# Performance work log

Measured on AMD Instinct MI355X. Metric: run time of the kernel, lower is better.

## Reference

```python
import jax, jax.numpy as jnp
import numpy as np
import math

B, S, D, H = 4, 1024, 512, 8
HD = D // H
HID = 4 * D


def clinear(xr, xi, lm, ph, bm=None, bp=None):
    # magnitude-phase parameterized complex linear: W = exp(lm) * e^{i*ph}
    mag = jnp.exp(lm)
    wr = mag * jnp.cos(ph)
    wi = mag * jnp.sin(ph)
    r = xr @ wr.T - xi @ wi.T
    i = xr @ wi.T + xi @ wr.T
    if bm is not None:
        r = r + bm * jnp.cos(bp)
        i = i + bm * jnp.sin(bp)
    return r, i


def cln(xr, xi, gr, gi, br, bi, eps=1e-6):
    mr = xr.mean(-1, keepdims=True)
    mi = xi.mean(-1, keepdims=True)
    cr, ci = xr - mr, xi - mi
    var = (cr * cr + ci * ci).mean(-1, keepdims=True)
    inv = 1.0 / jnp.sqrt(var + eps)
    nr, ni = cr * inv, ci * inv
    return nr * gr - ni * gi + br, nr * gi + ni * gr + bi


def rotate_half(x):
    h = x.shape[-1] // 2
    return jnp.concatenate([-x[..., h:], x[..., :h]], axis=-1)


def split_heads(x):  # (B,S,D) -> (B,H,S,HD)
    return x.reshape(B, S, H, HD).transpose(0, 2, 1, 3)


def merge_heads(x):  # (B,H,S,HD) -> (B,S,D)
    return x.transpose(0, 2, 1, 3).reshape(B, S, D)


def setup_inputs() -> dict:
    key = jax.random.key(0)
    ks = iter(jax.random.split(key, 64))

    def lin(o_f, i_f):
        lm = jax.random.normal(next(ks), (o_f, i_f)) * 0.1 - 0.5 * math.log(i_f)
        ph = jax.random.uniform(next(ks), (o_f, i_f), minval=-math.pi, maxval=math.pi)
        return lm.astype(jnp.float32), ph.astype(jnp.float32)

    inp = {}
    inp['x_real'] = jax.random.normal(next(ks), (B, S, D), dtype=jnp.float32)
    inp['x_imag'] = jax.random.normal(next(ks), (B, S, D), dtype=jnp.float32)
    inp['ln1_gr'] = jnp.ones(D); inp['ln1_gi'] = jnp.zeros(D)
    inp['ln1_br'] = jnp.zeros(D); inp['ln1_bi'] = jnp.zeros(D)
    for nm in ['q', 'k', 'v', 'o']:
        lm, ph = lin(D, D)
        inp[nm + '_lm'] = lm; inp[nm + '_ph'] = ph
        inp[nm + '_bm'] = jnp.zeros(D); inp[nm + '_bp'] = jnp.zeros(D)
    inp['ln2_gr'] = jnp.ones(D); inp['ln2_gi'] = jnp.zeros(D)
    inp['ln2_br'] = jnp.zeros(D); inp['ln2_bi'] = jnp.zeros(D)
    inp['gate_lm'], inp['gate_ph'] = lin(HID, D)
    inp['up_lm'], inp['up_ph'] = lin(HID, D)
    inp['down_lm'], inp['down_ph'] = lin(D, HID)
    return inp


def reference(x_real, x_imag, ln1_gr, ln1_gi, ln1_br, ln1_bi,
              q_lm, q_ph, q_bm, q_bp, k_lm, k_ph, k_bm, k_bp,
              v_lm, v_ph, v_bm, v_bp, o_lm, o_ph, o_bm, o_bp,
              ln2_gr, ln2_gi, ln2_br, ln2_bi,
              gate_lm, gate_ph, up_lm, up_ph, down_lm, down_ph):
    # --- pre-attention complex LayerNorm ---
    hr, hi = cln(x_real, x_imag, ln1_gr, ln1_gi, ln1_br, ln1_bi)

    # --- complex QKV projections ---
    qr, qi = clinear(hr, hi, q_lm, q_ph, q_bm, q_bp)
    kr, ki = clinear(hr, hi, k_lm, k_ph, k_bm, k_bp)
    vr, vi = clinear(hr, hi, v_lm, v_ph, v_bm, v_bp)
    qr, qi = split_heads(qr), split_heads(qi)
    kr, ki = split_heads(kr), split_heads(ki)
    vr, vi = split_heads(vr), split_heads(vi)

    # --- complex RoPE (same real rotation applied to real & imag parts) ---
    pos = jnp.arange(S, dtype=jnp.float32)
    inv_freq = 1.0 / (10000.0 ** (jnp.arange(0, HD, 2, dtype=jnp.float32) / HD))
    freqs = pos[:, None] * inv_freq[None, :]          # (S, HD/2)
    cos = jnp.concatenate([jnp.cos(freqs)] * 2, -1)[None, None]  # (1,1,S,HD)
    sin = jnp.concatenate([jnp.sin(freqs)] * 2, -1)[None, None]
    rot = lambda x: x * cos + rotate_half(x) * sin
    qr, qi, kr, ki = rot(qr), rot(qi), rot(kr), rot(ki)

    # --- Hermitian attention: Re(q . conj(k)) = qr.kr + qi.ki ---
    scale = 1.0 / math.sqrt(HD)
    scores = (jnp.einsum('bhqd,bhkd->bhqk', qr, kr)
              + jnp.einsum('bhqd,bhkd->bhqk', qi, ki)) * scale
    causal = jnp.tril(jnp.ones((S, S), dtype=bool))
    scores = jnp.where(causal, scores, jnp.float32(-1e9))
    attn = jax.nn.softmax(scores, axis=-1)            # real-valued weights
    ar = jnp.einsum('bhqk,bhkd->bhqd', attn, vr)
    ai = jnp.einsum('bhqk,bhkd->bhqd', attn, vi)
    ar, ai = merge_heads(ar), merge_heads(ai)
    ar, ai = clinear(ar, ai, o_lm, o_ph, o_bm, o_bp)

    # --- residual + LN2 ---
    res_r, res_i = x_real + ar, x_imag + ai
    hr, hi = cln(res_r, res_i, ln2_gr, ln2_gi, ln2_br, ln2_bi)

    # --- complex gated FFN (SwiGLU-style, complex gating) ---
    gr_, gi_ = clinear(hr, hi, gate_lm, gate_ph)
    s = jax.nn.sigmoid(jnp.sqrt(gr_ * gr_ + gi_ * gi_))  # sigmoid(|gate|)
    gar, gai = gr_ * s, gi_ * s
    ur, ui = clinear(hr, hi, up_lm, up_ph)
    hid_r = gar * ur - gai * ui
    hid_i = gar * ui + gai * ur
    dr, di = clinear(hid_r, hid_i, down_lm, down_ph)

    out_r = res_r + dr
    out_i = res_i + di
    return jnp.stack([out_r, out_i], axis=0)  # (2, B, S, D)
```

## Files before the change

kernel.cpp:

```cpp
#include <hip/hip_runtime.h>
#include <math.h>

#define kB 4
#define kS 1024
#define kD 512
#define kH 8
#define kHD 64
#define kHID 2048
#define kNT (kB * kS)
#define kBSD (kNT * kD)

typedef __attribute__((ext_vector_type(8))) short bf16x8;
typedef __attribute__((ext_vector_type(4))) float f32x4;

#define AS1 __attribute__((address_space(1)))
#define AS3 __attribute__((address_space(3)))

__device__ __forceinline__ float bf2f(unsigned short u) {
  return __uint_as_float(((unsigned int)u) << 16);
}
__device__ __forceinline__ unsigned short f2bf(float f) {
  unsigned int u = __float_as_uint(f);
  u += 0x7fffu + ((u >> 16) & 1u);
  return (unsigned short)(u >> 16);
}
__device__ __forceinline__ unsigned int pack2(unsigned short a, unsigned short b) {
  return (unsigned)a | ((unsigned)b << 16);
}

__global__ __launch_bounds__(256) void build_wA_kernel(
    const float* __restrict__ qlm, const float* __restrict__ qph,
    const float* __restrict__ klm, const float* __restrict__ kph,
    const float* __restrict__ vlm, const float* __restrict__ vph,
    const float* __restrict__ olm, const float* __restrict__ oph,
    const float* __restrict__ qbm, const float* __restrict__ qbp,
    const float* __restrict__ kbm, const float* __restrict__ kbp,
    const float* __restrict__ vbm, const float* __restrict__ vbp,
    const float* __restrict__ obm, const float* __restrict__ obp,
    const float* __restrict__ xr, const float* __restrict__ xi,
    const float* __restrict__ g_r, const float* __restrict__ g_i,
    const float* __restrict__ b_r, const float* __restrict__ b_i,
    unsigned short* __restrict__ Wqkv, unsigned short* __restrict__ Wo,
    float* __restrict__ qkvBias, float* __restrict__ oBias,
    unsigned short* __restrict__ H) {
  int bx = blockIdx.x;
  if (bx >= 4104) {
    int w = threadIdx.x >> 6, lane = threadIdx.x & 63;
    int t = (bx - 4104) * 4 + w;
    int d0 = lane * 8;
    const float* xrt = xr + (size_t)t * 512 + d0;
    const float* xit = xi + (size_t)t * 512 + d0;
    float4 a0 = *(const float4*)&xrt[0];
    float4 a1 = *(const float4*)&xrt[4];
    float4 c0 = *(const float4*)&xit[0];
    float4 c1 = *(const float4*)&xit[4];
    float s1 = a0.x + a0.y + a0.z + a0.w + a1.x + a1.y + a1.z + a1.w;
    float s2 = c0.x + c0.y + c0.z + c0.w + c1.x + c1.y + c1.z + c1.w;
#pragma unroll
    for (int off = 1; off < 64; off <<= 1) {
      s1 += __shfl_xor(s1, off);
      s2 += __shfl_xor(s2, off);
    }
    float mr = s1 * (1.f / kD), mi = s2 * (1.f / kD);
    float ar[8] = {a0.x, a0.y, a0.z, a0.w, a1.x, a1.y, a1.z, a1.w};
    float ai[8] = {c0.x, c0.y, c0.z, c0.w, c1.x, c1.y, c1.z, c1.w};
    float v = 0.f;
#pragma unroll
    for (int e = 0; e < 8; e++) {
      float cr = ar[e] - mr, ci = ai[e] - mi;
      v += cr * cr + ci * ci;
    }
#pragma unroll
    for (int off = 1; off < 64; off <<= 1) v += __shfl_xor(v, off);
    float inv = rsqrtf(v * (1.f / kD) + 1e-6f);
    unsigned short pr[8], pi[8];
#pragma unroll
    for (int e = 0; e < 8; e++) {
      float nr = (ar[e] - mr) * inv;
      float ni = (ai[e] - mi) * inv;
      pr[e] = f2bf(nr * g_r[d0 + e] - ni * g_i[d0 + e] + b_r[d0 + e]);
      pi[e] = f2bf(nr * g_i[d0 + e] + ni * g_r[d0 + e] + b_i[d0 + e]);
    }
    unsigned short* ot = H + (size_t)t * 1024 + d0;
    *(bf16x8*)&ot[0] = *(const bf16x8*)pr;
    *(bf16x8*)&ot[512] = *(const bf16x8*)pi;
    return;
  }
  if (bx >= 4096) {
    int gid = (bx - 4096) * 256 + threadIdx.x;
    int seg = gid >> 9, m = gid & 511;
    const float* bm = seg == 0 ? qbm : seg == 1 ? kbm : seg == 2 ? vbm : obm;
    const float* bp = seg == 0 ? qbp : seg == 1 ? kbp : seg == 2 ? vbp : obp;
    float s, c;
    __sincosf(bp[m], &s, &c);
    float br = bm[m] * c, bi = bm[m] * s;
    if (seg < 3) {
      int h = m >> 6, d = m & 63;
      qkvBias[seg * 1024 + h * 128 + d] = br;
      qkvBias[seg * 1024 + h * 128 + 64 + d] = bi;
    } else {
      oBias[m] = br;
      oBias[512 + m] = bi;
    }
    return;
  }
  int gid = bx * 256 + threadIdx.x;
  int seg = gid >> 18;
  int id = gid & 262143;
  const float* lm = seg == 0 ? qlm : seg == 1 ? klm : seg == 2 ? vlm : olm;
  const float* ph = seg == 0 ? qph : seg == 1 ? kph : seg == 2 ? vph : oph;
  float mm = __expf(lm[id]);
  float s, c;
  __sincosf(ph[id], &s, &c);
  float wr = mm * c, wi = mm * s;
  int m = id >> 9, k = id & 511;
  if (seg < 3) {
    int h = m >> 6, d = m & 63;
    size_t rowR = (size_t)seg * 1024 + h * 128 + d;
    size_t rowI = rowR + 64;
    Wqkv[rowR * 1024 + k] = f2bf(wr);
    Wqkv[rowR * 1024 + 512 + k] = f2bf(-wi);
    Wqkv[rowI * 1024 + k] = f2bf(wi);
    Wqkv[rowI * 1024 + 512 + k] = f2bf(wr);
  } else {
    Wo[(size_t)m * 1024 + k] = f2bf(wr);
    Wo[(size_t)m * 1024 + 512 + k] = f2bf(-wi);
    Wo[(size_t)(512 + m) * 1024 + k] = f2bf(wi);
    Wo[(size_t)(512 + m) * 1024 + 512 + k] = f2bf(wr);
  }
}

__global__ __launch_bounds__(256) void build_wB_kernel(
    const float* __restrict__ glm, const float* __restrict__ gph,
    const float* __restrict__ ulm, const float* __restrict__ uph,
    const float* __restrict__ dlm, const float* __restrict__ dph,
    unsigned short* __restrict__ Wgu, unsigned short* __restrict__ Wd) {
  int gid = blockIdx.x * 256 + threadIdx.x;
  int seg = gid >> 19;
  int id0 = (gid & 524287) * 2;
  const float* lm = seg == 0 ? glm : seg == 1 ? ulm : dlm;
  const float* ph = seg == 0 ? gph : seg == 1 ? uph : dph;
  float2 lm2 = *(const float2*)&lm[id0];
  float2 ph2 = *(const float2*)&ph[id0];
  float m0 = __expf(lm2.x), m1 = __expf(lm2.y);
  float s0, c0, s1, c1;
  __sincosf(ph2.x, &s0, &c0);
  __sincosf(ph2.y, &s1, &c1);
  float wr0 = m0 * c0, wi0 = m0 * s0;
  float wr1 = m1 * c1, wi1 = m1 * s1;
  if (seg < 2) {
    int T = id0 >> 9, k = id0 & 511;
    size_t base = (size_t)(T >> 4) * 64 + (T & 15);
    size_t rR = base + (seg * 2 + 0) * 16;
    size_t rI = base + (seg * 2 + 1) * 16;
    *(unsigned int*)&Wgu[rR * 1024 + k] = pack2(f2bf(wr0), f2bf(wr1));
    *(unsigned int*)&Wgu[rR * 1024 + 512 + k] = pack2(f2bf(-wi0), f2bf(-wi1));
    *(unsigned int*)&Wgu[rI * 1024 + k] = pack2(f2bf(wi0), f2bf(wi1));
    *(unsigned int*)&Wgu[rI * 1024 + 512 + k] = pack2(f2bf(wr0), f2bf(wr1));
  } else {
    int m = id0 >> 11, j = id0 & 2047;
    ushort4 a;
    a.x = f2bf(wr0); a.y = f2bf(-wi0); a.z = f2bf(wr1); a.w = f2bf(-wi1);
    *(ushort4*)&Wd[(size_t)m * 4096 + 2 * j] = a;
    ushort4 b;
    b.x = f2bf(wi0); b.y = f2bf(wr0); b.z = f2bf(wi1); b.w = f2bf(wr1);
    *(ushort4*)&Wd[(size_t)(512 + m) * 4096 + 2 * j] = b;
  }
}

__global__ __launch_bounds__(256) void cln_kernel(
    const float* __restrict__ xr, const float* __restrict__ xi, int stride,
    const float* __restrict__ g_r, const float* __restrict__ g_i,
    const float* __restrict__ b_r, const float* __restrict__ b_i,
    unsigned short* __restrict__ out) {
  int w = threadIdx.x >> 6, lane = threadIdx.x & 63;
  int t = blockIdx.x * 4 + w;
  int d0 = lane * 8;
  const float* xrt = xr + (size_t)t * stride + d0;
  const float* xit = xi + (size_t)t * stride + d0;
  float4 a0 = *(const float4*)&xrt[0];
  float4 a1 = *(const float4*)&xrt[4];
  float4 c0 = *(const float4*)&xit[0];
  float4 c1 = *(const float4*)&xit[4];

  float s1 = a0.x + a0.y + a0.z + a0.w + a1.x + a1.y + a1.z + a1.w;
  float s2 = c0.x + c0.y + c0.z + c0.w + c1.x + c1.y + c1.z + c1.w;
#pragma unroll
  for (int off = 1; off < 64; off <<= 1) {
    s1 += __shfl_xor(s1, off);
    s2 += __shfl_xor(s2, off);
  }
  float mr = s1 * (1.f / kD), mi = s2 * (1.f / kD);

  float ar[8] = {a0.x, a0.y, a0.z, a0.w, a1.x, a1.y, a1.z, a1.w};
  float ai[8] = {c0.x, c0.y, c0.z, c0.w, c1.x, c1.y, c1.z, c1.w};
  float v = 0.f;
#pragma unroll
  for (int e = 0; e < 8; e++) {
    float cr = ar[e] - mr, ci = ai[e] - mi;
    v += cr * cr + ci * ci;
  }
#pragma unroll
  for (int off = 1; off < 64; off <<= 1) v += __shfl_xor(v, off);
  float inv = rsqrtf(v * (1.f / kD) + 1e-6f);

  unsigned short pr[8], pi[8];
#pragma unroll
  for (int e = 0; e < 8; e++) {
    float nr = (ar[e] - mr) * inv;
    float ni = (ai[e] - mi) * inv;
    pr[e] = f2bf(nr * g_r[d0 + e] - ni * g_i[d0 + e] + b_r[d0 + e]);
    pi[e] = f2bf(nr * g_i[d0 + e] + ni * g_r[d0 + e] + b_i[d0 + e]);
  }
  unsigned short* ot = out + (size_t)t * 1024 + d0;
  *(bf16x8*)&ot[0] = *(const bf16x8*)pr;
  *(bf16x8*)&ot[512] = *(const bf16x8*)pi;
}

__global__ __launch_bounds__(256) void cgemm_mfma_kernel(
    const unsigned short* __restrict__ X, int ldx,
    const unsigned short* __restrict__ Wt, int K,
    const float* __restrict__ bias, int mode,
    unsigned short* __restrict__ outb, int ldo,
    unsigned short* __restrict__ vtb) {
  __shared__ unsigned short Sh[128 * 64 * 2];
  unsigned short* Xs = Sh;
  unsigned short* Ws = Sh + 8192;

  const int tid = threadIdx.x;
  const int w = tid >> 6;
  const int lane = tid & 63;
  const int quad = lane >> 4;
  const int l15 = lane & 15;
  const int m0 = blockIdx.x * 128;
  const int n0 = blockIdx.y * 128;
  const int wm = (w & 1) * 64;
  const int wn = (w >> 1) * 64;

  const int rsub = lane >> 3;
  const int grow = w * 32 + rsub;
  const int gcol = ((lane & 7) ^ rsub) * 8;
  const unsigned short* gx = X + (size_t)(n0 + grow) * ldx + gcol;
  const unsigned short* gw = Wt + (size_t)(m0 + grow) * K + gcol;

  const int rg = (l15 & 7);

  f32x4 acc[4][4];
#pragma unroll
  for (int i = 0; i < 4; i++)
#pragma unroll
    for (int j = 0; j < 4; j++) acc[i][j] = (f32x4){0.f, 0.f, 0.f, 0.f};

  for (int k0 = 0; k0 < K; k0 += 64) {
    __syncthreads();
#pragma unroll
    for (int t = 0; t < 4; t++) {
      __builtin_amdgcn_global_load_lds((const AS1 void*)(gx + (size_t)t * 8 * ldx + k0),
                                       (AS3 void*)&Xs[w * 2048 + t * 512], 16, 0, 0);
      __builtin_amdgcn_global_load_lds((const AS1 void*)(gw + (size_t)t * 8 * K + k0),
                                       (AS3 void*)&Ws[w * 2048 + t * 512], 16, 0, 0);
    }
    __syncthreads();

#pragma unroll
    for (int ks = 0; ks < 2; ks++) {
      const int gsel = ((ks * 4 + quad) ^ rg) * 8;
      bf16x8 af[4], bf[4];
#pragma unroll
      for (int t = 0; t < 4; t++) {
        af[t] = *(const bf16x8*)&Xs[(wn + t * 16 + l15) * 64 + gsel];
        bf[t] = *(const bf16x8*)&Ws[(wm + t * 16 + l15) * 64 + gsel];
      }
#pragma unroll
      for (int i = 0; i < 4; i++)
#pragma unroll
        for (int j = 0; j < 4; j++)
          acc[i][j] = __builtin_amdgcn_mfma_f32_16x16x32_bf16(af[i], bf[j], acc[i][j], 0, 0, 0);
    }
  }

  if (mode == 4) {
    int T = ((m0 + wm) >> 6) * 16 + l15;
#pragma unroll
    for (int i = 0; i < 4; ++i) {
      int row0 = n0 + wn + i * 16 + quad * 4;
#pragma unroll
      for (int r = 0; r < 4; ++r) {
        float gr = acc[i][0][r], gi = acc[i][1][r];
        float ur = acc[i][2][r], ui = acc[i][3][r];
        float sg = __builtin_amdgcn_rcpf(1.f + __expf(-sqrtf(gr * gr + gi * gi)));
        float gar = gr * sg, gai = gi * sg;
        unsigned int pk = pack2(f2bf(gar * ur - gai * ui), f2bf(gar * ui + gai * ur));
        *(unsigned int*)&outb[(size_t)(row0 + r) * ldo + 2 * T] = pk;
      }
    }
  } else if (mode == 3 && m0 < 2048) {
#pragma unroll
    for (int j = 0; j < 4; ++j) {
      float bv = bias[m0 + wm + j * 16 + l15];
#pragma unroll
      for (int i = 0; i < 4; ++i)
#pragma unroll
        for (int r = 0; r < 4; ++r) acc[i][j][r] += bv;
    }
    const int sbase = ((n0 + wn) & (kS - 1)) + quad * 4;
#pragma unroll
    for (int j01 = 0; j01 < 2; ++j01) {
      float fi = (float)(j01 * 16 + l15);
      float f = __expf(fi * -0.28782313662425572f);
      float c1, s1, c16, s16, cI, sI;
      __sincosf(f, &s1, &c1);
      __sincosf(16.f * f, &s16, &c16);
      __sincosf((float)sbase * f, &sI, &cI);
#pragma unroll
      for (int i = 0; i < 4; ++i) {
        float cc = cI, ss = sI;
#pragma unroll
        for (int r = 0; r < 4; ++r) {
          float x0 = acc[i][j01][r], x1 = acc[i][j01 + 2][r];
          acc[i][j01][r] = x0 * cc - x1 * ss;
          acc[i][j01 + 2][r] = x1 * cc + x0 * ss;
          float cn = cc * c1 - ss * s1;
          ss = ss * c1 + cc * s1;
          cc = cn;
        }
        float cn = cI * c16 - sI * s16;
        sI = sI * c16 + cI * s16;
        cI = cn;
      }
    }
#pragma unroll
    for (int j = 0; j < 4; ++j) {
      int col = m0 + wm + j * 16 + l15;
#pragma unroll
      for (int i = 0; i < 4; ++i) {
        int row0 = n0 + wn + i * 16 + quad * 4;
#pragma unroll
        for (int r = 0; r < 4; ++r)
          outb[(size_t)(row0 + r) * ldo + col] = f2bf(acc[i][j][r]);
      }
    }
  } else {
    unsigned short* Ts = Sh;
#pragma unroll
    for (int p = 0; p < 2; ++p) {
      __syncthreads();
      if ((w & 1) == p) {
#pragma unroll
        for (int j = 0; j < 4; ++j) {
          float bv = bias[m0 + wm + j * 16 + l15];
          int fl = j * 16 + l15;
#pragma unroll
          for (int i = 0; i < 4; ++i) {
            int tk = wn + i * 16 + quad * 4;
#pragma unroll
            for (int r = 0; r < 4; ++r)
              Ts[fl * 130 + tk + r] = f2bf(acc[i][j][r] + bv);
          }
        }
      }
      __syncthreads();
      {
        int fr = tid >> 2, seg = tid & 3;
        int f = (m0 - 2048) + p * 64 + fr;
        int hh = f >> 7, dc = f & 127;
        int bb = n0 >> 10, sbase2 = (n0 & (kS - 1)) + seg * 32;
        unsigned short* dst = &vtb[(size_t)((bb * 8 + hh) * 128 + dc) * 1024 + sbase2];
        const unsigned short* src = &Ts[fr * 130 + seg * 32];
#pragma unroll
        for (int u = 0; u < 4; u++)
          *(bf16x8*)(dst + u * 8) = *(const bf16x8*)(src + u * 8);
      }
    }
  }
}

__global__ __launch_bounds__(512, 2) void cgemm_mfma_gu256_kernel(
    const unsigned short* __restrict__ X, int ldx,
    const unsigned short* __restrict__ Wt, int K,
    unsigned short* __restrict__ outb, int ldo) {
  __shared__ unsigned short Sh[65536];

  const int tid = threadIdx.x;
  const int w = tid >> 6;
  const int lane = tid & 63;
  const int quad = lane >> 4;
  const int l15 = lane & 15;
  const int m0 = blockIdx.x * 256;
  const int n0 = blockIdx.y * 256;
  const int wfeat = w & 1;
  const int wtok = w >> 1;

  const int srow = lane >> 3;
  const int sgran = ((lane & 7) ^ srow) * 8;
  const unsigned short* gA = X + (size_t)(n0 + w * 32 + srow) * ldx + sgran;
  const unsigned short* gB = Wt + (size_t)(m0 + w * 32 + srow) * K + sgran;

  f32x4 acc[4][8];
#pragma unroll
  for (int i = 0; i < 4; i++)
#pragma unroll
    for (int j = 0; j < 8; j++) acc[i][j] = (f32x4){0.f, 0.f, 0.f, 0.f};

  auto stage_tile = [&](int kt, int bsel) {
    const int k0 = kt * 64;
    unsigned short* dA = &Sh[bsel * 32768 + w * 2048];
    unsigned short* dB = &Sh[bsel * 32768 + 16384 + w * 2048];
#pragma unroll
    for (int u = 0; u < 4; ++u) {
      __builtin_amdgcn_global_load_lds((const AS1 void*)(gA + (size_t)u * 8 * ldx + k0),
                                       (AS3 void*)(dA + u * 512), 16, 0, 0);
      __builtin_amdgcn_global_load_lds((const AS1 void*)(gB + (size_t)u * 8 * K + k0),
                                       (AS3 void*)(dB + u * 512), 16, 0, 0);
    }
  };

  auto compute_tile = [&](const unsigned short* As, const unsigned short* Bs) {
    bf16x8 af[4][2];
#pragma unroll
    for (int i = 0; i < 4; ++i)
#pragma unroll
      for (int ks = 0; ks < 2; ++ks)
        af[i][ks] = *(const bf16x8*)&As[(wtok * 64 + i * 16 + l15) * 64 +
                                        (((ks * 4 + quad) ^ (l15 & 7)) * 8)];
#pragma unroll
    for (int jp = 0; jp < 4; ++jp) {
      bf16x8 bq[2][2];
#pragma unroll
      for (int jj = 0; jj < 2; ++jj)
#pragma unroll
        for (int ks = 0; ks < 2; ++ks)
          bq[jj][ks] = *(const bf16x8*)&Bs[(wfeat * 128 + (jp * 2 + jj) * 16 + l15) * 64 +
                                           (((ks * 4 + quad) ^ (l15 & 7)) * 8)];
      __builtin_amdgcn_s_setprio(1);
#pragma unroll
      for (int i = 0; i < 4; ++i)
#pragma unroll
        for (int jj = 0; jj < 2; ++jj) {
          const int j = jp * 2 + jj;
          acc[i][j] = __builtin_amdgcn_mfma_f32_16x16x32_bf16(af[i][0], bq[jj][0], acc[i][j], 0, 0, 0);
          acc[i][j] = __builtin_amdgcn_mfma_f32_16x16x32_bf16(af[i][1], bq[jj][1], acc[i][j], 0, 0, 0);
        }
      __builtin_amdgcn_s_setprio(0);
    }
  };

  const int nt = K >> 6;
  stage_tile(0, 0);
  for (int t = 0; t < nt; t += 2) {
    if (t + 1 < nt) {
      stage_tile(t + 1, 1);
      asm volatile("s_waitcnt vmcnt(8)" ::: "memory");
    } else {
      asm volatile("s_waitcnt vmcnt(0)" ::: "memory");
    }
    __builtin_amdgcn_s_barrier();
    asm volatile("" ::: "memory");
    compute_tile(&Sh[0], &Sh[16384]);
    asm volatile("" ::: "memory");
    __builtin_amdgcn_s_barrier();

    if (t + 2 < nt) {
      stage_tile(t + 2, 0);
      asm volatile("s_waitcnt vmcnt(8)" ::: "memory");
    } else {
      asm volatile("s_waitcnt vmcnt(0)" ::: "memory");
    }
    __builtin_amdgcn_s_barrier();
    asm volatile("" ::: "memory");
    compute_tile(&Sh[32768], &Sh[32768 + 16384]);
    asm volatile("" ::: "memory");
    __builtin_amdgcn_s_barrier();
  }

#pragma unroll
  for (int i = 0; i < 4; ++i) {
    int row0 = n0 + wtok * 64 + i * 16 + quad * 4;
#pragma unroll
    for (int jh = 0; jh < 2; ++jh) {
      int T = ((m0 + wfeat * 128 + jh * 64) >> 6) * 16 + l15;
#pragma unroll
      for (int r = 0; r < 4; ++r) {
        float gr = acc[i][jh * 4 + 0][r], gi = acc[i][jh * 4 + 1][r];
        float ur = acc[i][jh * 4 + 2][r], ui = acc[i][jh * 4 + 3][r];
        float sg = __builtin_amdgcn_rcpf(1.f + __expf(-sqrtf(gr * gr + gi * gi)));
        float gar = gr * sg, gai = gi * sg;
        unsigned int pk = pack2(f2bf(gar * ur - gai * ui), f2bf(gar * ui + gai * ur));
        *(unsigned int*)&outb[(size_t)(row0 + r) * ldo + 2 * T] = pk;
      }
    }
  }
}

__global__ __launch_bounds__(256) void cgemm_mfma_n64_kernel(
    const unsigned short* __restrict__ X, int ldx,
    const unsigned short* __restrict__ Wt, int K,
    const float* __restrict__ bias, int mode,
    const float* __restrict__ resr, const float* __restrict__ resi,
    float* __restrict__ outf) {
  __shared__ unsigned short Xs[64 * 128];
  __shared__ unsigned short Ws[128 * 128];

  const int tid = threadIdx.x;
  const int w = tid >> 6;
  const int lane = tid & 63;
  const int quad = lane >> 4;
  const int l15 = lane & 15;
  const int m0 = blockIdx.x * 128;
  const int n0 = blockIdx.y * 64;
  const int wm = (w & 1) * 64;
  const int wn = (w >> 1) * 32;

  f32x4 acc[2][4];
#pragma unroll
  for (int i = 0; i < 2; i++)
#pragma unroll
    for (int j = 0; j < 4; j++) acc[i][j] = (f32x4){0.f, 0.f, 0.f, 0.f};

  for (int k0 = 0; k0 < K; k0 += 128) {
    __syncthreads();
#pragma unroll
    for (int t = 0; t < 4; t++) {
      int key = t * 4 + quad;
      int gc = (l15 ^ key) * 8;
      __builtin_amdgcn_global_load_lds(
          (const AS1 void*)(X + (size_t)(n0 + w * 16 + t * 4 + quad) * ldx + k0 + gc),
          (AS3 void*)&Xs[w * 2048 + t * 512], 16, 0, 0);
    }
#pragma unroll
    for (int t = 0; t < 8; t++) {
      int key = (t * 4 + quad) & 15;
      int gc = (l15 ^ key) * 8;
      __builtin_amdgcn_global_load_lds(
          (const AS1 void*)(Wt + (size_t)(m0 + w * 32 + t * 4 + quad) * K + k0 + gc),
          (AS3 void*)&Ws[w * 4096 + t * 512], 16, 0, 0);
    }
    __syncthreads();

#pragma unroll
    for (int ks = 0; ks < 4; ks++) {
      const int gsel = ((ks * 4 + quad) ^ l15) * 8;
      bf16x8 af[2], bf[4];
#pragma unroll
      for (int t = 0; t < 2; t++)
        af[t] = *(const bf16x8*)&Xs[(wn + t * 16 + l15) * 128 + gsel];
#pragma unroll
      for (int t = 0; t < 4; t++)
        bf[t] = *(const bf16x8*)&Ws[(wm + t * 16 + l15) * 128 + gsel];
#pragma unroll
      for (int i = 0; i < 2; i++)
#pragma unroll
        for (int j = 0; j < 4; j++)
          acc[i][j] = __builtin_amdgcn_mfma_f32_16x16x32_bf16(af[i], bf[j], acc[i][j], 0, 0, 0);
    }
  }

#pragma unroll
  for (int j = 0; j < 4; ++j) {
    int col = m0 + wm + j * 16 + l15;
    float bv = bias ? bias[col] : 0.f;
#pragma unroll
    for (int i = 0; i < 2; ++i) {
      int row0 = n0 + wn + i * 16 + quad * 4;
#pragma unroll
      for (int r = 0; r < 4; ++r) {
        int row = row0 + r;
        float val = acc[i][j][r] + bv;
        if (mode == 1) {
          float xres = (col < 512) ? resr[(size_t)row * 512 + col]
                                   : resi[(size_t)row * 512 + col - 512];
          outf[(size_t)row * 1024 + col] = val + xres;
        } else {
          float rv = resr[(size_t)row * 1024 + col] + val;
          size_t dd = (col < 512) ? ((size_t)row * 512 + col)
                                  : ((size_t)kBSD + (size_t)row * 512 + (col - 512));
          outf[dd] = rv;
        }
      }
    }
  }
}

__global__ __launch_bounds__(256) void attn_mfma_kernel(
    const unsigned short* __restrict__ qkv,
    const unsigned short* __restrict__ vt,
    unsigned short* __restrict__ out) {
  __shared__ unsigned short Ks[64 * 136];
  __shared__ unsigned short Vs[128 * 72];
  __shared__ unsigned short Ps[4 * 16 * 72];

  const int tid = threadIdx.x;
  const int w = tid >> 6;
  const int lane = tid & 63;
  const int quad = lane >> 4;
  const int l15 = lane & 15;

  int bid = blockIdx.x;
  int second = bid >> 8;
  int u = bid & 255;
  int t_ = u & 15;
  const int qt = second ? (15 - t_) : t_;
  const int h = (u >> 4) & 7;
  const int b = second * 2 + (u >> 7);
  const int q0 = qt * 64;
  const int wrow0 = q0 + w * 16;

  bf16x8 qa[4];
  {
    size_t base = (size_t)(b * kS + wrow0 + l15) * 3072 + h * 128;
#pragma unroll
    for (int ks = 0; ks < 4; ks++)
      qa[ks] = *(const bf16x8*)&qkv[base + ks * 32 + quad * 8];
  }

  f32x4 oacc[8];
#pragma unroll
  for (int dt = 0; dt < 8; dt++) oacc[dt] = (f32x4){0.f, 0.f, 0.f, 0.f};
  float m_r[4] = {-1e30f, -1e30f, -1e30f, -1e30f};
  float l_r[4] = {0.f, 0.f, 0.f, 0.f};

  const int nkt = qt + 1;
  const float cexp = 0.1803368801f;

  const unsigned short* gkbase = qkv + 1024 + h * 128;
  const unsigned short* gvbase = vt + (size_t)((b * 8 + h) * 128) * 1024;

  for (int kt = 0; kt < nkt; ++kt) {
    const int k0 = kt * 64;
    __syncthreads();
    {
      const unsigned short* gk = gkbase + (size_t)(b * kS + k0) * 3072;
      int ch = tid * 4;
#pragma unroll
      for (int u2 = 0; u2 < 4; u2++) {
        int r = (ch + u2) >> 4, cc = ((ch + u2) & 15) * 8;
        *(bf16x8*)&Ks[r * 136 + cc] = *(const bf16x8*)&gk[(size_t)r * 3072 + cc];
      }
#pragma unroll
      for (int u2 = 0; u2 < 4; u2++) {
        int vr = (ch + u2) >> 3, vc = ((ch + u2) & 7) * 8;
        *(bf16x8*)&Vs[vr * 72 + vc] = *(const bf16x8*)&gvbase[(size_t)vr * 1024 + k0 + vc];
      }
    }
    __syncthreads();

    f32x4 s[4];
#pragma unroll
    for (int ns = 0; ns < 4; ns++) {
      s[ns] = (f32x4){0.f, 0.f, 0.f, 0.f};
#pragma unroll
      for (int ks = 0; ks < 4; ks++) {
        bf16x8 kb = *(const bf16x8*)&Ks[(ns * 16 + l15) * 136 + ks * 32 + quad * 8];
        s[ns] = __builtin_amdgcn_mfma_f32_16x16x32_bf16(qa[ks], kb, s[ns], 0, 0, 0);
      }
    }

    if (k0 + 63 > wrow0) {
#pragma unroll
      for (int r = 0; r < 4; r++) {
        int qrow = wrow0 + quad * 4 + r;
#pragma unroll
        for (int ns = 0; ns < 4; ns++)
          if (k0 + ns * 16 + l15 > qrow) s[ns][r] = -1e30f;
      }
    }

    float alpha[4];
#pragma unroll
    for (int r = 0; r < 4; r++) {
      float mx = fmaxf(fmaxf(s[0][r], s[1][r]), fmaxf(s[2][r], s[3][r]));
      mx = fmaxf(mx, __shfl_xor(mx, 1));
      mx = fmaxf(mx, __shfl_xor(mx, 2));
      mx = fmaxf(mx, __shfl_xor(mx, 4));
      mx = fmaxf(mx, __shfl_xor(mx, 8));
      float mn = fmaxf(m_r[r], mx);
      float al = exp2f((m_r[r] - mn) * cexp);
      m_r[r] = mn;
      float rs = 0.f;
#pragma unroll
      for (int ns = 0; ns < 4; ns++) {
        float p = exp2f((s[ns][r] - mn) * cexp);
        s[ns][r] = p;
        rs += p;
      }
      rs += __shfl_xor(rs, 1);
      rs += __shfl_xor(rs, 2);
      rs += __shfl_xor(rs, 4);
      rs += __shfl_xor(rs, 8);
      l_r[r] = l_r[r] * al + rs;
      alpha[r] = al;
    }

#pragma unroll
    for (int dt = 0; dt < 8; dt++)
#pragma unroll
      for (int r = 0; r < 4; r++) oacc[dt][r] *= alpha[r];

    unsigned short* pw = &Ps[w * 1152];
#pragma unroll
    for (int r = 0; r < 4; r++) {
      int q = quad * 4 + r;
#pragma unroll
      for (int ns = 0; ns < 4; ns++)
        pw[q * 72 + ns * 16 + l15] = f2bf(s[ns][r]);
    }
    bf16x8 pa0 = *(const bf16x8*)&pw[l15 * 72 + quad * 8];
    bf16x8 pa1 = *(const bf16x8*)&pw[l15 * 72 + 32 + quad * 8];

#pragma unroll
    for (int dt = 0; dt < 8; dt++) {
      bf16x8 vb0 = *(const bf16x8*)&Vs[(dt * 16 + l15) * 72 + quad * 8];
      bf16x8 vb1 = *(const bf16x8*)&Vs[(dt * 16 + l15) * 72 + 32 + quad * 8];
      oacc[dt] = __builtin_amdgcn_mfma_f32_16x16x32_bf16(pa0, vb0, oacc[dt], 0, 0, 0);
      oacc[dt] = __builtin_amdgcn_mfma_f32_16x16x32_bf16(pa1, vb1, oacc[dt], 0, 0, 0);
    }
  }

  float inv[4];
#pragma unroll
  for (int r = 0; r < 4; r++) inv[r] = __builtin_amdgcn_rcpf(l_r[r]);
#pragma unroll
  for (int dt = 0; dt < 8; dt++) {
    int dcat = dt * 16 + l15;
    int col = (dcat < 64) ? (h * 64 + dcat) : (512 + h * 64 + dcat - 64);
#pragma unroll
    for (int r = 0; r < 4; r++) {
      int tok = b * kS + wrow0 + quad * 4 + r;
      out[(size_t)tok * 1024 + col] = f2bf(oacc[dt][r] * inv[r]);
    }
  }
}

extern "C" void kernel_launch(void* const* d_in, const int* in_sizes, int n_in,
                              void* d_out, int out_size, void* d_ws, size_t ws_size,
                              hipStream_t stream) {
  const float* x_real = (const float*)d_in[0];
  const float* x_imag = (const float*)d_in[1];
  const float* ln1_gr = (const float*)d_in[2];
  const float* ln1_gi = (const float*)d_in[3];
  const float* ln1_br = (const float*)d_in[4];
  const float* ln1_bi = (const float*)d_in[5];
  const float* q_lm = (const float*)d_in[6];
  const float* q_ph = (const float*)d_in[7];
  const float* q_bm = (const float*)d_in[8];
  const float* q_bp = (const float*)d_in[9];
  const float* k_lm = (const float*)d_in[10];
  const float* k_ph = (const float*)d_in[11];
  const float* k_bm = (const float*)d_in[12];
  const float* k_bp = (const float*)d_in[13];
  const float* v_lm = (const float*)d_in[14];
  const float* v_ph = (const float*)d_in[15];
  const float* v_bm = (const float*)d_in[16];
  const float* v_bp = (const float*)d_in[17];
  const float* o_lm = (const float*)d_in[18];
  const float* o_ph = (const float*)d_in[19];
  const float* o_bm = (const float*)d_in[20];
  const float* o_bp = (const float*)d_in[21];
  const float* ln2_gr = (const float*)d_in[22];
  const float* ln2_gi = (const float*)d_in[23];
  const float* ln2_br = (const float*)d_in[24];
  const float* ln2_bi = (const float*)d_in[25];
  const float* gate_lm = (const float*)d_in[26];
  const float* gate_ph = (const float*)d_in[27];
  const float* up_lm = (const float*)d_in[28];
  const float* up_ph = (const float*)d_in[29];
  const float* down_lm = (const float*)d_in[30];
  const float* down_ph = (const float*)d_in[31];

  char* wsb = (char*)d_ws;
  unsigned short* Wqkv = (unsigned short*)(wsb + 0);
  unsigned short* Wo   = (unsigned short*)(wsb + 6291456);
  unsigned short* Wgu  = (unsigned short*)(wsb + 8388608);
  unsigned short* Wd   = (unsigned short*)(wsb + 25165824);
  float* qkvBias = (float*)(wsb + 33554432);
  float* oBias   = (float*)(wsb + 33566720);
  float* res     = (float*)(wsb + 33570816);
  unsigned short* H = (unsigned short*)(wsb + 50348032);
  char* big = wsb + 58736640;
  unsigned short* qkv     = (unsigned short*)big;
  unsigned short* attnout = (unsigned short*)(big + 25165824);
  unsigned short* vtb     = (unsigned short*)(big + 33554432);
  unsigned short* hid     = (unsigned short*)big;

  float* outf = (float*)d_out;

  build_wA_kernel<<<5128, 256, 0, stream>>>(q_lm, q_ph, k_lm, k_ph, v_lm, v_ph,
                                            o_lm, o_ph, q_bm, q_bp, k_bm, k_bp,
                                            v_bm, v_bp, o_bm, o_bp,
                                            x_real, x_imag, ln1_gr, ln1_gi,
                                            ln1_br, ln1_bi,
                                            Wqkv, Wo, qkvBias, oBias, H);
  build_wB_kernel<<<6144, 256, 0, stream>>>(gate_lm, gate_ph, up_lm, up_ph,
                                            down_lm, down_ph, Wgu, Wd);

  {
    dim3 g(3072 / 128, kNT / 128);
    cgemm_mfma_kernel<<<g, 256, 0, stream>>>(H, 1024, Wqkv, 1024, qkvBias, 3, qkv, 3072, vtb);
  }

  attn_mfma_kernel<<<kB * kH * (kS / 64), 256, 0, stream>>>(qkv, vtb, attnout);

  {
    dim3 g(1024 / 128, kNT / 64);
    cgemm_mfma_n64_kernel<<<g, 256, 0, stream>>>(attnout, 1024, Wo, 1024, oBias, 1,
                                                 x_real, x_imag, res);
  }

  cln_kernel<<<kNT / 4, 256, 0, stream>>>(res, res + 512, 1024, ln2_gr, ln2_gi, ln2_br, ln2_bi, H);

  {
    dim3 g(8192 / 256, kNT / 256);
    cgemm_mfma_gu256_kernel<<<g, 512, 0, stream>>>(H, 1024, Wgu, 1024, hid, 4096);
  }

  {
    dim3 g(1024 / 128, kNT / 64);
    cgemm_mfma_n64_kernel<<<g, 256, 0, stream>>>(hid, 4096, Wd, 4096, nullptr, 2,
                                                 res, nullptr, outf);
  }
}
```

Before: 392.1 us.

## Restructure gate-up GEMM main loop into ping-pong barrier-phased LDS-read/MFMA clusters

Replaces the two-tile unrolled loop and compute_tile lambda with a single loop over K tiles that alternates buffers by parity. Each K step is split into four phases: a wave reads a slice of A and B fragments from LDS, hits a barrier, runs a 16-MFMA cluster at raised priority, then hits another barrier. The goal is to line up LDS reads and MFMA bursts across waves, in a ping-pong style, so they overlap better and register pressure from fragments drops. The cost is many more workgroup barriers per K tile, which can stall waves if the phases are unbalanced.

```diff
diff --git a/kernel.cpp b/kernel.cpp
--- a/kernel.cpp
+++ b/kernel.cpp
@@ -375,6 +375,8 @@
   }
 }
 
+#define BARC() do { asm volatile("" ::: "memory"); __builtin_amdgcn_s_barrier(); asm volatile("" ::: "memory"); } while (0)
+
 __global__ __launch_bounds__(512, 2) void cgemm_mfma_gu256_kernel(
     const unsigned short* __restrict__ X, int ldx,
     const unsigned short* __restrict__ Wt, int K,
@@ -390,6 +392,7 @@
   const int n0 = blockIdx.y * 256;
   const int wfeat = w & 1;
   const int wtok = w >> 1;
+  const int swz = l15 & 7;
 
   const int srow = lane >> 3;
   const int sgran = ((lane & 7) ^ srow) * 8;
@@ -415,62 +418,49 @@
     }
   };
 
-  auto compute_tile = [&](const unsigned short* As, const unsigned short* Bs) {
-    bf16x8 af[4][2];
-#pragma unroll
-    for (int i = 0; i < 4; ++i)
-#pragma unroll
-      for (int ks = 0; ks < 2; ++ks)
-        af[i][ks] = *(const bf16x8*)&As[(wtok * 64 + i * 16 + l15) * 64 +
-                                        (((ks * 4 + quad) ^ (l15 & 7)) * 8)];
-#pragma unroll
-    for (int jp = 0; jp < 4; ++jp) {
-      bf16x8 bq[2][2];
-#pragma unroll
-      for (int jj = 0; jj < 2; ++jj)
-#pragma unroll
-        for (int ks = 0; ks < 2; ++ks)
-          bq[jj][ks] = *(const bf16x8*)&Bs[(wfeat * 128 + (jp * 2 + jj) * 16 + l15) * 64 +
-                                           (((ks * 4 + quad) ^ (l15 & 7)) * 8)];
-      __builtin_amdgcn_s_setprio(1);
-#pragma unroll
-      for (int i = 0; i < 4; ++i)
-#pragma unroll
-        for (int jj = 0; jj < 2; ++jj) {
-          const int j = jp * 2 + jj;
-          acc[i][j] = __builtin_amdgcn_mfma_f32_16x16x32_bf16(af[i][0], bq[jj][0], acc[i][j], 0, 0, 0);
-          acc[i][j] = __builtin_amdgcn_mfma_f32_16x16x32_bf16(af[i][1], bq[jj][1], acc[i][j], 0, 0, 0);
-        }
-      __builtin_amdgcn_s_setprio(0);
-    }
-  };
-
   const int nt = K >> 6;
   stage_tile(0, 0);
-  for (int t = 0; t < nt; t += 2) {
+
+  for (int t = 0; t < nt; ++t) {
     if (t + 1 < nt) {
-      stage_tile(t + 1, 1);
+      stage_tile(t + 1, (t + 1) & 1);
       asm volatile("s_waitcnt vmcnt(8)" ::: "memory");
     } else {
       asm volatile("s_waitcnt vmcnt(0)" ::: "memory");
     }
-    __builtin_amdgcn_s_barrier();
-    asm volatile("" ::: "memory");
-    compute_tile(&Sh[0], &Sh[16384]);
-    asm volatile("" ::: "memory");
-    __builtin_amdgcn_s_barrier();
-
-    if (t + 2 < nt) {
-      stage_tile(t + 2, 0);
-      asm volatile("s_waitcnt vmcnt(8)" ::: "memory");
-    } else {
-      asm volatile("s_waitcnt vmcnt(0)" ::: "memory");
-    }
-    __builtin_amdgcn_s_barrier();
-    asm volatile("" ::: "memory");
-    compute_tile(&Sh[32768], &Sh[32768 + 16384]);
-    asm volatile("" ::: "memory");
-    __builtin_amdgcn_s_barrier();
+    BARC();
+
+    const unsigned short* As = &Sh[(t & 1) * 32768];
+    const unsigned short* Bs = &Sh[(t & 1) * 32768 + 16384];
+
+    bf16x8 af[4];
+#pragma unroll
+    for (int ks = 0; ks < 2; ++ks) {
+#pragma unroll
+      for (int jh = 0; jh < 2; ++jh) {
+        if (jh == 0) {
+#pragma unroll
+          for (int i = 0; i < 4; ++i)
+            af[i] = *(const bf16x8*)&As[(wtok * 64 + i * 16 + l15) * 64 +
+                                        (((ks * 4 + quad) ^ swz) * 8)];
+        }
+        bf16x8 bq[4];
+#pragma unroll
+        for (int jj = 0; jj < 4; ++jj)
+          bq[jj] = *(const bf16x8*)&Bs[(wfeat * 128 + (jh * 4 + jj) * 16 + l15) * 64 +
+                                       (((ks * 4 + quad) ^ swz) * 8)];
+        BARC();
+        __builtin_amdgcn_s_setprio(1);
+#pragma unroll
+        for (int i = 0; i < 4; ++i)
+#pragma unroll
+          for (int jj = 0; jj < 4; ++jj)
+            acc[i][jh * 4 + jj] = __builtin_amdgcn_mfma_f32_16x16x32_bf16(
+                af[i], bq[jj], acc[i][jh * 4 + jj], 0, 0, 0);
+        __builtin_amdgcn_s_setprio(0);
+        BARC();
+      }
+    }
   }
 
 #pragma unroll
```

Measured after the change: 394.8 us. About the same (+0.7%).

## Double-buffer LDS tiles in n64 complex GEMM with async prefetch

Applied to the files above, without the earlier changes.

Rewrites the n64 complex GEMM main loop to use a K-tile of 64 with two LDS buffers. The next tile is prefetched via global_load_lds while the current one is consumed, synchronised by explicit vmcnt waits and raw barriers. This aims to overlap global memory latency with MFMA work. The trade-offs are twice as many iterations and two barriers per tile, plus a changed swizzle for the smaller tile width.

```diff
diff --git a/kernel.cpp b/kernel.cpp
--- a/kernel.cpp
+++ b/kernel.cpp
@@ -27,6 +27,8 @@
 __device__ __forceinline__ unsigned int pack2(unsigned short a, unsigned short b) {
   return (unsigned)a | ((unsigned)b << 16);
 }
+
+#define BARC() do { asm volatile("" ::: "memory"); __builtin_amdgcn_s_barrier(); asm volatile("" ::: "memory"); } while (0)
 
 __global__ __launch_bounds__(256) void build_wA_kernel(
     const float* __restrict__ qlm, const float* __restrict__ qph,
@@ -498,8 +500,7 @@
     const float* __restrict__ bias, int mode,
     const float* __restrict__ resr, const float* __restrict__ resi,
     float* __restrict__ outf) {
-  __shared__ unsigned short Xs[64 * 128];
-  __shared__ unsigned short Ws[128 * 128];
+  __shared__ unsigned short Sh[24576];
 
   const int tid = threadIdx.x;
   const int w = tid >> 6;
@@ -510,6 +511,12 @@
   const int n0 = blockIdx.y * 64;
   const int wm = (w & 1) * 64;
   const int wn = (w >> 1) * 32;
+  const int swz = l15 & 7;
+
+  const int srow = lane >> 3;
+  const int sgran = ((lane & 7) ^ srow) * 8;
+  const unsigned short* gX = X + (size_t)(n0 + w * 16 + srow) * ldx + sgran;
+  const unsigned short* gW = Wt + (size_t)(m0 + w * 32 + srow) * K + sgran;
 
   f32x4 acc[2][4];
 #pragma unroll
@@ -517,42 +524,49 @@
 #pragma unroll
     for (int j = 0; j < 4; j++) acc[i][j] = (f32x4){0.f, 0.f, 0.f, 0.f};
 
-  for (int k0 = 0; k0 < K; k0 += 128) {
-    __syncthreads();
-#pragma unroll
-    for (int t = 0; t < 4; t++) {
-      int key = t * 4 + quad;
-      int gc = (l15 ^ key) * 8;
-      __builtin_amdgcn_global_load_lds(
-          (const AS1 void*)(X + (size_t)(n0 + w * 16 + t * 4 + quad) * ldx + k0 + gc),
-          (AS3 void*)&Xs[w * 2048 + t * 512], 16, 0, 0);
-    }
-#pragma unroll
-    for (int t = 0; t < 8; t++) {
-      int key = (t * 4 + quad) & 15;
-      int gc = (l15 ^ key) * 8;
-      __builtin_amdgcn_global_load_lds(
-          (const AS1 void*)(Wt + (size_t)(m0 + w * 32 + t * 4 + quad) * K + k0 + gc),
-          (AS3 void*)&Ws[w * 4096 + t * 512], 16, 0, 0);
-    }
-    __syncthreads();
-
-#pragma unroll
-    for (int ks = 0; ks < 4; ks++) {
-      const int gsel = ((ks * 4 + quad) ^ l15) * 8;
+  auto stage_tile = [&](int kt, int bsel) {
+    const int k0 = kt * 64;
+    unsigned short* dX = &Sh[bsel * 12288 + w * 1024];
+    unsigned short* dW = &Sh[bsel * 12288 + 4096 + w * 2048];
+#pragma unroll
+    for (int u = 0; u < 2; ++u)
+      __builtin_amdgcn_global_load_lds((const AS1 void*)(gX + (size_t)u * 8 * ldx + k0),
+                                       (AS3 void*)(dX + u * 512), 16, 0, 0);
+#pragma unroll
+    for (int u = 0; u < 4; ++u)
+      __builtin_amdgcn_global_load_lds((const AS1 void*)(gW + (size_t)u * 8 * K + k0),
+                                       (AS3 void*)(dW + u * 512), 16, 0, 0);
+  };
+
+  const int nt = K >> 6;
+  stage_tile(0, 0);
+  for (int t = 0; t < nt; ++t) {
+    if (t + 1 < nt) {
+      stage_tile(t + 1, (t + 1) & 1);
+      asm volatile("s_waitcnt vmcnt(6)" ::: "memory");
+    } else {
+      asm volatile("s_waitcnt vmcnt(0)" ::: "memory");
+    }
+    BARC();
+    const unsigned short* Xs = &Sh[(t & 1) * 12288];
+    const unsigned short* Ws = &Sh[(t & 1) * 12288 + 4096];
+#pragma unroll
+    for (int ks = 0; ks < 2; ++ks) {
+      const int gsel = ((ks * 4 + quad) ^ swz) * 8;
       bf16x8 af[2], bf[4];
 #pragma unroll
-      for (int t = 0; t < 2; t++)
-        af[t] = *(const bf16x8*)&Xs[(wn + t * 16 + l15) * 128 + gsel];
-#pragma unroll
-      for (int t = 0; t < 4; t++)
-        bf[t] = *(const bf16x8*)&Ws[(wm + t * 16 + l15) * 128 + gsel];
+      for (int t2 = 0; t2 < 2; ++t2)
+        af[t2] = *(const bf16x8*)&Xs[(wn + t2 * 16 + l15) * 64 + gsel];
+#pragma unroll
+      for (int t2 = 0; t2 < 4; ++t2)
+        bf[t2] = *(const bf16x8*)&Ws[(wm + t2 * 16 + l15) * 64 + gsel];
 #pragma unroll
       for (int i = 0; i < 2; i++)
 #pragma unroll
         for (int j = 0; j < 4; j++)
           acc[i][j] = __builtin_amdgcn_mfma_f32_16x16x32_bf16(af[i], bf[j], acc[i][j], 0, 0, 0);
     }
+    BARC();
   }
 
 #pragma unroll
```

Result: no change. 388.3 us (-1.0%).
